# Kernel optimization log

Measured on AMD Instinct MI355X. Metric: run time of the kernel, lower is better.

## Reference

```python
import jax, jax.numpy as jnp
import numpy as np
from jax import lax

B, T, H = 32768, 64, 16
VOCAB_USER = 600001
VOCAB_LAUNCH = 3


def setup_inputs() -> dict:
    key = jax.random.key(0)
    ks = jax.random.split(key, 10)
    s = 1.0 / np.sqrt(H)
    return {
        "user_id": jax.random.randint(ks[0], (B,), 0, VOCAB_USER),
        "launch_seq": jax.random.randint(ks[1], (B, T), 0, VOCAB_LAUNCH),
        "user_emb": jax.random.normal(ks[2], (VOCAB_USER, H), dtype=jnp.float32),
        "launch_emb": jax.random.normal(ks[3], (VOCAB_LAUNCH, H), dtype=jnp.float32),
        "W_ih": jax.random.uniform(ks[4], (3 * H, H), jnp.float32, -s, s),
        "W_hh": jax.random.uniform(ks[5], (3 * H, H), jnp.float32, -s, s),
        "b_ih": jax.random.uniform(ks[6], (3 * H,), jnp.float32, -s, s),
        "b_hh": jax.random.uniform(ks[7], (3 * H,), jnp.float32, -s, s),
        "fc_W": jax.random.uniform(ks[8], (1, 2 * H), jnp.float32, -s, s),
        "fc_b": jax.random.uniform(ks[9], (1,), jnp.float32, -s, s),
    }


def reference(user_id, launch_seq, user_emb, launch_emb, W_ih, W_hh, b_ih, b_hh, fc_W, fc_b):
    u = user_emb[user_id]                      # (B, H)
    x = launch_emb[launch_seq]                 # (B, T, H)
    # precompute input contributions to the gates for all timesteps
    gx_all = jnp.einsum('bth,gh->btg', x, W_ih) + b_ih  # (B, T, 3H)

    def step(h, gx):
        gh = h @ W_hh.T + b_hh                 # (B, 3H)
        r = jax.nn.sigmoid(gx[:, :H] + gh[:, :H])
        z = jax.nn.sigmoid(gx[:, H:2 * H] + gh[:, H:2 * H])
        n = jnp.tanh(gx[:, 2 * H:] + r * gh[:, 2 * H:])
        h_new = (1.0 - z) * n + z * h
        return h_new, h_new

    h0 = jnp.zeros((x.shape[0], H), dtype=x.dtype)
    _, hs = lax.scan(step, h0, jnp.swapaxes(gx_all, 0, 1))  # hs: (T, B, H)
    pooled = jnp.mean(hs, axis=0)              # (B, H)
    fc_in = jnp.concatenate([u, pooled], axis=1)  # (B, 2H)
    return fc_in @ fc_W.T + fc_b               # (B, 1)
```

## Files before the change

### kernel.cpp

```cpp
#include <hip/hip_runtime.h>
#include <hip/hip_bf16.h>
#include <string.h>


#define NBLK 1024

typedef __attribute__((ext_vector_type(8))) short    short8;
typedef __attribute__((ext_vector_type(4))) float    floatx4;
typedef __attribute__((ext_vector_type(4))) unsigned uintx4;

static __device__ __forceinline__ float fexp2(float x) { return __builtin_amdgcn_exp2f(x); }
static __device__ __forceinline__ float frcp(float x)  { return __builtin_amdgcn_rcpf(x); }
static __device__ __forceinline__ unsigned short bfrne(float f) {
    union { __hip_bfloat16 b; unsigned short u; } cv; cv.b = __float2bfloat16(f); return cv.u;
}
static __device__ __forceinline__ float bf2f(unsigned short u) {
    unsigned v = ((unsigned)u) << 16; float f; memcpy(&f, &v, 4); return f;
}
static __device__ __forceinline__ unsigned pkbf(float a, float b) {
    return (unsigned)bfrne(a) | ((unsigned)bfrne(b) << 16);
}
static __device__ __forceinline__ float sel3(int c, float a0, float a1, float a2) {
    return c == 0 ? a0 : (c == 1 ? a1 : a2);
}

__global__ __launch_bounds__(64) void gru_mfma(
    const int* __restrict__ user_id,
    const int* __restrict__ launch_seq,
    const float* __restrict__ user_emb,
    const float* __restrict__ launch_emb,
    const float* __restrict__ W_ih,
    const float* __restrict__ W_hh,
    const float* __restrict__ b_ih,
    const float* __restrict__ b_hh,
    const float* __restrict__ fc_W,
    const float* __restrict__ fc_b,
    float* __restrict__ out)
{
    constexpr float L  = 1.4426950408889634f;
    constexpr float L2 = 2.8853900817779268f;

    __shared__ float         gxlut[144];
    __shared__ unsigned char seqT[2048];

    const int tid  = threadIdx.x;
    const int col  = tid & 15;
    const int quad = tid >> 4;
    const bool isq2 = (quad == 2);
    const long long sampBase = (long long)blockIdx.x * 32;

    {
        int r = tid >> 1, w = tid & 1;
        const int* sp = launch_seq + (sampBase + r) * 64 + w * 32;
        #pragma unroll
        for (int g = 0; g < 8; ++g) {
            int4 v = ((const int4*)sp)[g];
            int t0 = w * 32 + g * 4;
            seqT[(t0 + 0) * 32 + r] = (unsigned char)v.x;
            seqT[(t0 + 1) * 32 + r] = (unsigned char)v.y;
            seqT[(t0 + 2) * 32 + r] = (unsigned char)v.z;
            seqT[(t0 + 3) * 32 + r] = (unsigned char)v.w;
        }
    }

    for (int idx = tid; idx < 144; idx += 64) {
        int s = idx / 48, g = idx - s * 48;
        float dot = b_ih[g];
        #pragma unroll
        for (int k = 0; k < 16; ++k)
            dot = fmaf(W_ih[g * 16 + k], launch_emb[s * 16 + k], dot);
        int gate = g >> 4, dim = g & 15;
        gxlut[(gate * 3 + s) * 16 + dim] =
            (g < 32) ? (-L * (dot + b_hh[g])) : (L2 * dot);
    }

    __syncthreads();

    short8 Wrh, Wrl, Wzh, Wzl, Wnh, Wnl;
    {
        auto makeW = [&](int goff, float scale, const float* gx3, float extra19,
                         short8& Hi, short8& Lo) {
            float w[8];
            #pragma unroll
            for (int j = 0; j < 8; ++j) w[j] = 0.f;
            if (quad < 2) {
                const float* row = W_hh + (goff + col) * 16 + quad * 8;
                #pragma unroll
                for (int j = 0; j < 8; ++j) w[j] = scale * row[j];
            } else if (quad == 2) {
                if (gx3) { w[0] = gx3[col]; w[1] = gx3[16 + col]; w[2] = gx3[32 + col]; }
                w[3] = extra19;
            }
            uintx4 hi, lo;
            #pragma unroll
            for (int p = 0; p < 4; ++p) {
                unsigned short h0 = bfrne(w[2 * p]), h1 = bfrne(w[2 * p + 1]);
                hi[p] = (unsigned)h0 | ((unsigned)h1 << 16);
                lo[p] = pkbf(w[2 * p] - bf2f(h0), w[2 * p + 1] - bf2f(h1));
            }
            Hi = __builtin_bit_cast(short8, hi);
            Lo = __builtin_bit_cast(short8, lo);
        };
        makeW(0,  -L, &gxlut[0],  0.f,                  Wrh, Wrl);
        makeW(16, -L, &gxlut[48], 0.f,                  Wzh, Wzl);
        makeW(32,  L2, (const float*)0, L2 * b_hh[32 + col], Wnh, Wnl);
    }

    floatx4 gn0 = *(const floatx4*)&gxlut[(6 + 0) * 16 + quad * 4];
    floatx4 gn1 = *(const floatx4*)&gxlut[(6 + 1) * 16 + quad * 4];
    floatx4 gn2 = *(const floatx4*)&gxlut[(6 + 2) * 16 + quad * 4];

    const int a1 = (col + 32 * (quad & 1)) * 4;
    const int a2 = a1 + 64;

    floatx4 hL = {0,0,0,0}, poolL = {0,0,0,0};
    floatx4 hR = {0,0,0,0}, poolR = {0,0,0,0};
    int cL = seqT[col];
    int cR = seqT[16 + col];
    short8 BL, BR;
    {
        unsigned P0 = (cL == 0 ? 0x3F80u : 0u) | (cL == 1 ? 0x3F800000u : 0u);
        unsigned P1 = (cL == 2 ? 0x3F80u : 0u) | 0x3F800000u;
        uintx4 b = {isq2 ? P0 : 0u, isq2 ? P1 : 0u, 0u, 0u};
        BL = __builtin_bit_cast(short8, b);
        P0 = (cR == 0 ? 0x3F80u : 0u) | (cR == 1 ? 0x3F800000u : 0u);
        P1 = (cR == 2 ? 0x3F80u : 0u) | 0x3F800000u;
        uintx4 b2 = {isq2 ? P0 : 0u, isq2 ? P1 : 0u, 0u, 0u};
        BR = __builtin_bit_cast(short8, b2);
    }

    const floatx4 CZ = {0.f, 0.f, 0.f, 0.f};

    auto step = [&](floatx4& h, floatx4& pool, short8& B, int& c, int base, int t) {
        floatx4 accr = __builtin_amdgcn_mfma_f32_16x16x32_bf16(Wrh, B, CZ, 0, 0, 0);
        floatx4 accz = __builtin_amdgcn_mfma_f32_16x16x32_bf16(Wzh, B, CZ, 0, 0, 0);
        floatx4 accn = __builtin_amdgcn_mfma_f32_16x16x32_bf16(Wnh, B, CZ, 0, 0, 0);
        accr = __builtin_amdgcn_mfma_f32_16x16x32_bf16(Wrl, B, accr, 0, 0, 0);
        accz = __builtin_amdgcn_mfma_f32_16x16x32_bf16(Wzl, B, accz, 0, 0, 0);
        accn = __builtin_amdgcn_mfma_f32_16x16x32_bf16(Wnl, B, accn, 0, 0, 0);

        int cn = seqT[((t + 1) & 63) * 32 + base + col];

        #pragma unroll
        for (int i = 0; i < 4; ++i) {
            float gnv = sel3(c, gn0[i], gn1[i], gn2[i]);
            float r  = frcp(1.0f + fexp2(accr[i]));
            float z  = frcp(1.0f + fexp2(accz[i]));
            float y  = fmaf(r, accn[i], gnv);
            float n  = fmaf(-2.0f, frcp(1.0f + fexp2(y)), 1.0f);
            float hn = fmaf(z, h[i] - n, n);
            h[i] = hn;
            pool[i] += hn;
        }

        unsigned hp0 = pkbf(h[0], h[1]);
        unsigned hp1 = pkbf(h[2], h[3]);
        unsigned P0 = (cn == 0 ? 0x3F80u : 0u) | (cn == 1 ? 0x3F800000u : 0u);
        unsigned P1 = (cn == 2 ? 0x3F80u : 0u) | 0x3F800000u;
        uintx4 b;
        b[0] = (unsigned)__builtin_amdgcn_ds_bpermute(a1, (int)hp0);
        b[1] = (unsigned)__builtin_amdgcn_ds_bpermute(a1, (int)hp1);
        b[2] = (unsigned)__builtin_amdgcn_ds_bpermute(a2, (int)hp0);
        b[3] = (unsigned)__builtin_amdgcn_ds_bpermute(a2, (int)hp1);
        b[0] = isq2 ? P0 : b[0];
        b[1] = isq2 ? P1 : b[1];
        B = __builtin_bit_cast(short8, b);
        c = cn;
    };

    #pragma unroll 2
    for (int t = 0; t < 64; ++t) {
        step(hL, poolL, BL, cL, 0, t);
        step(hR, poolR, BR, cR, 16, t);
    }

    float4 fc1 = *(const float4*)&fc_W[quad * 4];
    float4 fc2 = *(const float4*)&fc_W[16 + quad * 4];
    const float inv64 = 1.0f / 64.0f;
    #pragma unroll
    for (int chain = 0; chain < 2; ++chain) {
        const floatx4& pool = chain ? poolR : poolL;
        long long s = sampBase + chain * 16 + col;
        int uid = user_id[s];
        float4 u4 = *(const float4*)&user_emb[(long long)uid * 16 + quad * 4];
        float val = fc1.x * u4.x + fc1.y * u4.y + fc1.z * u4.z + fc1.w * u4.w;
        val = fmaf(fc2.x * inv64, pool[0], val);
        val = fmaf(fc2.y * inv64, pool[1], val);
        val = fmaf(fc2.z * inv64, pool[2], val);
        val = fmaf(fc2.w * inv64, pool[3], val);
        val += __shfl_xor(val, 16);
        val += __shfl_xor(val, 32);
        if (quad == 0) out[s] = val + fc_b[0];
    }
}

extern "C" void kernel_launch(void* const* d_in, const int* in_sizes, int n_in,
                              void* d_out, int out_size, void* d_ws, size_t ws_size,
                              hipStream_t stream) {
    const int*   user_id    = (const int*)d_in[0];
    const int*   launch_seq = (const int*)d_in[1];
    const float* user_emb   = (const float*)d_in[2];
    const float* launch_emb = (const float*)d_in[3];
    const float* W_ih       = (const float*)d_in[4];
    const float* W_hh       = (const float*)d_in[5];
    const float* b_ih       = (const float*)d_in[6];
    const float* b_hh       = (const float*)d_in[7];
    const float* fc_W       = (const float*)d_in[8];
    const float* fc_b       = (const float*)d_in[9];
    float* out = (float*)d_out;

    gru_mfma<<<dim3(NBLK), dim3(64), 0, stream>>>(
        user_id, launch_seq, user_emb, launch_emb,
        W_ih, W_hh, b_ih, b_hh, fc_W, fc_b, out);
}
```

Measured before the change: 133.7 us.

## Interleave four independent GRU chains per wave with register-packed sequence codes

Each 64-thread block now handles 64 samples as four independent recurrent chains instead of two, and the grid shrinks to 512 blocks. Interleaving more chains is meant to hide MFMA and transcendental latency within one wave. The launch sequence is packed into 2-bit codes held in registers and redistributed with ds_bpermute, replacing the shared-memory transpose and the per-step LDS loads. In exchange, register pressure rises and there are half as many waves available to fill the GPU.

```diff
diff --git a/kernel.cpp b/kernel.cpp
--- a/kernel.cpp
+++ b/kernel.cpp
@@ -3,7 +3,7 @@
 #include <string.h>
 
 
-#define NBLK 1024
+#define NBLK 512
 
 typedef __attribute__((ext_vector_type(8))) short    short8;
 typedef __attribute__((ext_vector_type(4))) float    floatx4;
@@ -40,26 +40,29 @@
     constexpr float L  = 1.4426950408889634f;
     constexpr float L2 = 2.8853900817779268f;
 
-    __shared__ float         gxlut[144];
-    __shared__ unsigned char seqT[2048];
+    __shared__ float gxlut[144];
 
     const int tid  = threadIdx.x;
     const int col  = tid & 15;
     const int quad = tid >> 4;
     const bool isq2 = (quad == 2);
-    const long long sampBase = (long long)blockIdx.x * 32;
-
+    const long long sampBase = (long long)blockIdx.x * 64;
+
+    unsigned pk[4];
     {
-        int r = tid >> 1, w = tid & 1;
-        const int* sp = launch_seq + (sampBase + r) * 64 + w * 32;
-        #pragma unroll
-        for (int g = 0; g < 8; ++g) {
-            int4 v = ((const int4*)sp)[g];
-            int t0 = w * 32 + g * 4;
-            seqT[(t0 + 0) * 32 + r] = (unsigned char)v.x;
-            seqT[(t0 + 1) * 32 + r] = (unsigned char)v.y;
-            seqT[(t0 + 2) * 32 + r] = (unsigned char)v.z;
-            seqT[(t0 + 3) * 32 + r] = (unsigned char)v.w;
+        const int* sp = launch_seq + (sampBase + tid) * 64;
+        #pragma unroll
+        for (int w = 0; w < 4; ++w) {
+            unsigned p = 0;
+            #pragma unroll
+            for (int j = 0; j < 4; ++j) {
+                int4 v = ((const int4*)sp)[w * 4 + j];
+                p |= ((unsigned)v.x & 3u) << (2 * (4 * j + 0));
+                p |= ((unsigned)v.y & 3u) << (2 * (4 * j + 1));
+                p |= ((unsigned)v.z & 3u) << (2 * (4 * j + 2));
+                p |= ((unsigned)v.w & 3u) << (2 * (4 * j + 3));
+            }
+            pk[w] = p;
         }
     }
 
@@ -72,6 +75,15 @@
         int gate = g >> 4, dim = g & 15;
         gxlut[(gate * 3 + s) * 16 + dim] =
             (g < 32) ? (-L * (dot + b_hh[g])) : (L2 * dot);
+    }
+
+    unsigned sw[4][4];
+    #pragma unroll
+    for (int c = 0; c < 4; ++c) {
+        int addr = (16 * c + col) * 4;
+        #pragma unroll
+        for (int w = 0; w < 4; ++w)
+            sw[c][w] = (unsigned)__builtin_amdgcn_ds_bpermute(addr, (int)pk[w]);
     }
 
     __syncthreads();
@@ -113,81 +125,89 @@
     const int a1 = (col + 32 * (quad & 1)) * 4;
     const int a2 = a1 + 64;
 
-    floatx4 hL = {0,0,0,0}, poolL = {0,0,0,0};
-    floatx4 hR = {0,0,0,0}, poolR = {0,0,0,0};
-    int cL = seqT[col];
-    int cR = seqT[16 + col];
-    short8 BL, BR;
-    {
-        unsigned P0 = (cL == 0 ? 0x3F80u : 0u) | (cL == 1 ? 0x3F800000u : 0u);
-        unsigned P1 = (cL == 2 ? 0x3F80u : 0u) | 0x3F800000u;
+    floatx4 h[4], pool[4];
+    short8 B[4];
+    #pragma unroll
+    for (int c = 0; c < 4; ++c) {
+        h[c] = floatx4{0.f, 0.f, 0.f, 0.f};
+        pool[c] = floatx4{0.f, 0.f, 0.f, 0.f};
+        unsigned c0 = sw[c][0] & 3u;
+        unsigned P0 = (c0 == 0 ? 0x3F80u : 0u) | (c0 == 1 ? 0x3F800000u : 0u);
+        unsigned P1 = (c0 == 2 ? 0x3F80u : 0u) | 0x3F800000u;
         uintx4 b = {isq2 ? P0 : 0u, isq2 ? P1 : 0u, 0u, 0u};
-        BL = __builtin_bit_cast(short8, b);
-        P0 = (cR == 0 ? 0x3F80u : 0u) | (cR == 1 ? 0x3F800000u : 0u);
-        P1 = (cR == 2 ? 0x3F80u : 0u) | 0x3F800000u;
-        uintx4 b2 = {isq2 ? P0 : 0u, isq2 ? P1 : 0u, 0u, 0u};
-        BR = __builtin_bit_cast(short8, b2);
+        B[c] = __builtin_bit_cast(short8, b);
     }
 
     const floatx4 CZ = {0.f, 0.f, 0.f, 0.f};
 
-    auto step = [&](floatx4& h, floatx4& pool, short8& B, int& c, int base, int t) {
-        floatx4 accr = __builtin_amdgcn_mfma_f32_16x16x32_bf16(Wrh, B, CZ, 0, 0, 0);
-        floatx4 accz = __builtin_amdgcn_mfma_f32_16x16x32_bf16(Wzh, B, CZ, 0, 0, 0);
-        floatx4 accn = __builtin_amdgcn_mfma_f32_16x16x32_bf16(Wnh, B, CZ, 0, 0, 0);
-        accr = __builtin_amdgcn_mfma_f32_16x16x32_bf16(Wrl, B, accr, 0, 0, 0);
-        accz = __builtin_amdgcn_mfma_f32_16x16x32_bf16(Wzl, B, accz, 0, 0, 0);
-        accn = __builtin_amdgcn_mfma_f32_16x16x32_bf16(Wnl, B, accn, 0, 0, 0);
-
-        int cn = seqT[((t + 1) & 63) * 32 + base + col];
-
-        #pragma unroll
-        for (int i = 0; i < 4; ++i) {
-            float gnv = sel3(c, gn0[i], gn1[i], gn2[i]);
-            float r  = frcp(1.0f + fexp2(accr[i]));
-            float z  = frcp(1.0f + fexp2(accz[i]));
-            float y  = fmaf(r, accn[i], gnv);
-            float n  = fmaf(-2.0f, frcp(1.0f + fexp2(y)), 1.0f);
-            float hn = fmaf(z, h[i] - n, n);
-            h[i] = hn;
-            pool[i] += hn;
+    for (int w = 0; w < 4; ++w) {
+        unsigned cw[4], ncw[4];
+        #pragma unroll
+        for (int c = 0; c < 4; ++c) {
+            cw[c]  = sw[c][w];
+            ncw[c] = (sw[c][w] >> 2) | (w < 3 ? (sw[c][w + 1] << 30) : 0u);
         }
-
-        unsigned hp0 = pkbf(h[0], h[1]);
-        unsigned hp1 = pkbf(h[2], h[3]);
-        unsigned P0 = (cn == 0 ? 0x3F80u : 0u) | (cn == 1 ? 0x3F800000u : 0u);
-        unsigned P1 = (cn == 2 ? 0x3F80u : 0u) | 0x3F800000u;
-        uintx4 b;
-        b[0] = (unsigned)__builtin_amdgcn_ds_bpermute(a1, (int)hp0);
-        b[1] = (unsigned)__builtin_amdgcn_ds_bpermute(a1, (int)hp1);
-        b[2] = (unsigned)__builtin_amdgcn_ds_bpermute(a2, (int)hp0);
-        b[3] = (unsigned)__builtin_amdgcn_ds_bpermute(a2, (int)hp1);
-        b[0] = isq2 ? P0 : b[0];
-        b[1] = isq2 ? P1 : b[1];
-        B = __builtin_bit_cast(short8, b);
-        c = cn;
-    };
-
-    #pragma unroll 2
-    for (int t = 0; t < 64; ++t) {
-        step(hL, poolL, BL, cL, 0, t);
-        step(hR, poolR, BR, cR, 16, t);
+        #pragma unroll 4
+        for (int tt = 0; tt < 16; ++tt) {
+            floatx4 accr[4], accz[4], accn[4];
+            #pragma unroll
+            for (int c = 0; c < 4; ++c) {
+                accr[c] = __builtin_amdgcn_mfma_f32_16x16x32_bf16(Wrh, B[c], CZ, 0, 0, 0);
+                accz[c] = __builtin_amdgcn_mfma_f32_16x16x32_bf16(Wzh, B[c], CZ, 0, 0, 0);
+                accn[c] = __builtin_amdgcn_mfma_f32_16x16x32_bf16(Wnh, B[c], CZ, 0, 0, 0);
+            }
+            #pragma unroll
+            for (int c = 0; c < 4; ++c) {
+                accr[c] = __builtin_amdgcn_mfma_f32_16x16x32_bf16(Wrl, B[c], accr[c], 0, 0, 0);
+                accz[c] = __builtin_amdgcn_mfma_f32_16x16x32_bf16(Wzl, B[c], accz[c], 0, 0, 0);
+                accn[c] = __builtin_amdgcn_mfma_f32_16x16x32_bf16(Wnl, B[c], accn[c], 0, 0, 0);
+            }
+            #pragma unroll
+            for (int c = 0; c < 4; ++c) {
+                int cc = (int)(cw[c] & 3u);
+                #pragma unroll
+                for (int i = 0; i < 4; ++i) {
+                    float gnv = sel3(cc, gn0[i], gn1[i], gn2[i]);
+                    float r  = frcp(1.0f + fexp2(accr[c][i]));
+                    float z  = frcp(1.0f + fexp2(accz[c][i]));
+                    float y  = fmaf(r, accn[c][i], gnv);
+                    float n  = fmaf(-2.0f, frcp(1.0f + fexp2(y)), 1.0f);
+                    float hn = fmaf(z, h[c][i] - n, n);
+                    h[c][i] = hn;
+                    pool[c][i] += hn;
+                }
+                unsigned hp0 = pkbf(h[c][0], h[c][1]);
+                unsigned hp1 = pkbf(h[c][2], h[c][3]);
+                unsigned cn = ncw[c] & 3u;
+                unsigned P0 = (cn == 0 ? 0x3F80u : 0u) | (cn == 1 ? 0x3F800000u : 0u);
+                unsigned P1 = (cn == 2 ? 0x3F80u : 0u) | 0x3F800000u;
+                uintx4 b;
+                b[0] = (unsigned)__builtin_amdgcn_ds_bpermute(a1, (int)hp0);
+                b[1] = (unsigned)__builtin_amdgcn_ds_bpermute(a1, (int)hp1);
+                b[2] = (unsigned)__builtin_amdgcn_ds_bpermute(a2, (int)hp0);
+                b[3] = (unsigned)__builtin_amdgcn_ds_bpermute(a2, (int)hp1);
+                b[0] = isq2 ? P0 : b[0];
+                b[1] = isq2 ? P1 : b[1];
+                B[c] = __builtin_bit_cast(short8, b);
+                cw[c] >>= 2;
+                ncw[c] >>= 2;
+            }
+        }
     }
 
     float4 fc1 = *(const float4*)&fc_W[quad * 4];
     float4 fc2 = *(const float4*)&fc_W[16 + quad * 4];
     const float inv64 = 1.0f / 64.0f;
     #pragma unroll
-    for (int chain = 0; chain < 2; ++chain) {
-        const floatx4& pool = chain ? poolR : poolL;
-        long long s = sampBase + chain * 16 + col;
+    for (int c = 0; c < 4; ++c) {
+        long long s = sampBase + c * 16 + col;
         int uid = user_id[s];
         float4 u4 = *(const float4*)&user_emb[(long long)uid * 16 + quad * 4];
         float val = fc1.x * u4.x + fc1.y * u4.y + fc1.z * u4.z + fc1.w * u4.w;
-        val = fmaf(fc2.x * inv64, pool[0], val);
-        val = fmaf(fc2.y * inv64, pool[1], val);
-        val = fmaf(fc2.z * inv64, pool[2], val);
-        val = fmaf(fc2.w * inv64, pool[3], val);
+        val = fmaf(fc2.x * inv64, pool[c][0], val);
+        val = fmaf(fc2.y * inv64, pool[c][1], val);
+        val = fmaf(fc2.z * inv64, pool[c][2], val);
+        val = fmaf(fc2.w * inv64, pool[c][3], val);
         val += __shfl_xor(val, 16);
         val += __shfl_xor(val, 32);
         if (quad == 0) out[s] = val + fc_b[0];
```

Measured after the change: 171.4 us. 1.28x slower.
